# Kernel optimization log

Hardware: AMD Instinct MI355X
Metric: run time of the kernel (lower is better)

Reference implementation:

```python
import jax, jax.numpy as jnp
import numpy as np

D_MODEL = 768
N_HEADS = 12
HEAD_DIM = D_MODEL // N_HEADS
NEG = -10000.0


def setup_inputs() -> dict:
    key = jax.random.key(0)
    ks = jax.random.split(key, 8)
    B, S, D = 2, 2048, D_MODEL
    inp = {
        "q": jax.random.normal(ks[0], (B, S, D), dtype=jnp.float32),
        "k": jax.random.normal(ks[1], (B, S, D), dtype=jnp.float32),
        "v": jax.random.normal(ks[2], (B, S, D), dtype=jnp.float32),
        "attn_mask": jax.random.randint(ks[3], (B, S), 0, 2, dtype=jnp.int32),
        # weights stored [in, out]; apply as x @ W (equivalent to torch Linear)
        "Wq": jax.random.normal(ks[4], (D, D), dtype=jnp.float32) / np.sqrt(D),
        "Wk": jax.random.normal(ks[5], (D, D), dtype=jnp.float32) / np.sqrt(D),
        "Wv": jax.random.normal(ks[6], (D, D), dtype=jnp.float32) / np.sqrt(D),
        "Wo": jax.random.normal(ks[7], (D, D), dtype=jnp.float32) / np.sqrt(D),
        "mask_future": 1,
    }
    return inp


def reference(q, k, v, attn_mask, Wq, Wk, Wv, Wo, mask_future):
    B, S, D = q.shape
    H, hd = N_HEADS, HEAD_DIM
    # project and split heads -> [B, H, S, hd]
    qh = (q @ Wq).reshape(B, S, H, hd).transpose(0, 2, 1, 3)
    kh = (k @ Wk).reshape(B, S, H, hd).transpose(0, 2, 1, 3)
    vh = (v @ Wv).reshape(B, S, H, hd).transpose(0, 2, 1, 3)

    scale = 1.0 / np.sqrt(hd).astype(np.float32)
    # full [B, H, L, S] score matrix (naive SDPA, as in the original)
    scores = jnp.einsum("bhld,bhsd->bhls", qh, kh) * scale
    if mask_future:
        causal = jnp.triu(jnp.full((S, S), NEG, dtype=scores.dtype), k=1)
        scores = scores + causal
    # padding mask: [B, S] -> broadcast over heads and query positions
    pad = attn_mask[:, None, None, :] == 0
    scores = jnp.where(pad, NEG, scores)
    attn = jax.nn.softmax(scores, axis=-1)  # dropout p=0.0 -> identity
    out = jnp.einsum("bhls,bhsd->bhld", attn, vh)  # [B, H, L, hd]
    out = out.transpose(0, 2, 1, 3).reshape(B, S, D)
    return out @ Wo
```

## Files before the change

kernel.cpp:

```cpp
#include <hip/hip_runtime.h>


#define NEGV (-10000.0f)

typedef __attribute__((ext_vector_type(8))) short v8s;
typedef __attribute__((ext_vector_type(4))) float v4f;
typedef __attribute__((ext_vector_type(8))) unsigned short v8u;

#define GLDS16(g, l)                                            \
  __builtin_amdgcn_global_load_lds(                             \
      (const __attribute__((address_space(1))) void*)(g),       \
      (__attribute__((address_space(3))) void*)(l), 16, 0, 0)

__device__ __forceinline__ unsigned short f2bf(float f) {
  unsigned int u = __float_as_uint(f);
  u += 0x7FFFu + ((u >> 16) & 1u);
  return (unsigned short)(u >> 16);
}

__device__ __forceinline__ unsigned int cvt_pk_bf16(float lo, float hi) {
  unsigned int r;
  asm("v_cvt_pk_bf16_f32 %0, %1, %2" : "=v"(r) : "v"(lo), "v"(hi));
  return r;
}

__global__ __launch_bounds__(256) void transpose_w(
    const float* __restrict__ w0, const float* __restrict__ w1,
    const float* __restrict__ w2, const float* __restrict__ w3,
    unsigned short* __restrict__ t0, unsigned short* __restrict__ t1,
    unsigned short* __restrict__ t2, unsigned short* __restrict__ t3) {
  const float* w; unsigned short* t;
  switch (blockIdx.z) {
    case 0: w = w0; t = t0; break;
    case 1: w = w1; t = t1; break;
    case 2: w = w2; t = t2; break;
    default: w = w3; t = t3; break;
  }
  __shared__ unsigned short tile[32][33];
  const int tx = threadIdx.x & 31, ty = threadIdx.x >> 5;
  const int x0 = blockIdx.x * 32, y0 = blockIdx.y * 32;
#pragma unroll
  for (int j = 0; j < 4; j++)
    tile[ty + j * 8][tx] = f2bf(w[(size_t)(y0 + ty + j * 8) * 768 + x0 + tx]);
  __syncthreads();
#pragma unroll
  for (int j = 0; j < 4; j++)
    t[(size_t)(x0 + ty + j * 8) * 768 + y0 + tx] = tile[tx][ty + j * 8];
}

__global__ __launch_bounds__(256) void transpose_vh(
    const unsigned short* __restrict__ vh, unsigned short* __restrict__ vht) {
  __shared__ unsigned short tile[32][33];
  const size_t hoff = (size_t)blockIdx.z * 2048 * 64;
  const unsigned short* src = vh + hoff;
  unsigned short* dst = vht + hoff;
  const int s0 = blockIdx.x * 32, d0 = blockIdx.y * 32;
  const int tx = threadIdx.x & 31, ty = threadIdx.x >> 5;
#pragma unroll
  for (int j = 0; j < 4; j++)
    tile[ty + j * 8][tx] = src[(size_t)(s0 + ty + j * 8) * 64 + d0 + tx];
  __syncthreads();
#pragma unroll
  for (int j = 0; j < 4; j++)
    dst[(size_t)(d0 + ty + j * 8) * 2048 + s0 + tx] = tile[tx][ty + j * 8];
}

template <bool ABF16HEAD, bool CF32ROW>
__device__ __forceinline__ void gemm_core(const void* __restrict__ A,
                                          const unsigned short* __restrict__ Wt,
                                          void* __restrict__ C) {
  const int tid = threadIdx.x;
  const int wave = tid >> 6, lane = tid & 63;
  const int quad = lane >> 4, l16 = lane & 15;
  const int wm = wave >> 1, wn = wave & 1;
  const int bm = blockIdx.x * 128, bn = blockIdx.y * 128;

  __shared__ __align__(16) unsigned short As[128 * 32];
  __shared__ __align__(16) unsigned short Bs[128 * 32];

  v4f acc[4][4];
#pragma unroll
  for (int i = 0; i < 4; i++)
#pragma unroll
    for (int j = 0; j < 4; j++) acc[i][j] = (v4f){0.f, 0.f, 0.f, 0.f};

  for (int kt = 0; kt < 24; kt++) {
    __syncthreads();
#pragma unroll
    for (int p = 0; p < 2; p++) {
      int idx = p * 256 + tid;
      int r = idx >> 2, c0 = (idx & 3) << 3;
      int rg = bm + r, c = kt * 32 + c0;
      if (ABF16HEAD) {
        size_t aoff = ((size_t)((rg >> 11) * 12 + (c >> 6)) * 2048 +
                       (rg & 2047)) * 64 + (c & 63);
        GLDS16((const unsigned short*)A + aoff,
               &As[(size_t)(p * 256 + wave * 64) * 8]);
      } else {
        const float* Af = (const float*)A;
        size_t aoff = (size_t)rg * 768 + c;
        float4 x0 = *(const float4*)(Af + aoff);
        float4 x1 = *(const float4*)(Af + aoff + 4);
        v8u tmp;
        tmp[0] = f2bf(x0.x); tmp[1] = f2bf(x0.y);
        tmp[2] = f2bf(x0.z); tmp[3] = f2bf(x0.w);
        tmp[4] = f2bf(x1.x); tmp[5] = f2bf(x1.y);
        tmp[6] = f2bf(x1.z); tmp[7] = f2bf(x1.w);
        *(uint4*)&As[r * 32 + c0] = *(uint4*)&tmp;
      }
      GLDS16(&Wt[(size_t)(bn + r) * 768 + c],
             &Bs[(size_t)(p * 256 + wave * 64) * 8]);
    }
    __syncthreads();

    v8s aF[4], bF[4];
#pragma unroll
    for (int mt = 0; mt < 4; mt++)
      aF[mt] = *(const v8s*)&As[(wm * 64 + mt * 16 + l16) * 32 + quad * 8];
#pragma unroll
    for (int nt = 0; nt < 4; nt++)
      bF[nt] = *(const v8s*)&Bs[(wn * 64 + nt * 16 + l16) * 32 + quad * 8];
#pragma unroll
    for (int mt = 0; mt < 4; mt++)
#pragma unroll
      for (int nt = 0; nt < 4; nt++)
        acc[mt][nt] = __builtin_amdgcn_mfma_f32_16x16x32_bf16(
            aF[mt], bF[nt], acc[mt][nt], 0, 0, 0);
  }

#pragma unroll
  for (int mt = 0; mt < 4; mt++) {
#pragma unroll
    for (int i = 0; i < 4; i++) {
      int row = bm + wm * 64 + mt * 16 + quad * 4 + i;
#pragma unroll
      for (int nt = 0; nt < 4; nt++) {
        int col = bn + wn * 64 + nt * 16 + l16;
        if (CF32ROW) {
          ((float*)C)[(size_t)row * 768 + col] = acc[mt][nt][i];
        } else {
          size_t off = ((size_t)((row >> 11) * 12 + (col >> 6)) * 2048 +
                        (row & 2047)) * 64 + (col & 63);
          ((unsigned short*)C)[off] = f2bf(acc[mt][nt][i]);
        }
      }
    }
  }
}

__global__ __launch_bounds__(256) void gemm_qkv(
    const float* __restrict__ xq, const float* __restrict__ xk,
    const float* __restrict__ xv, const unsigned short* __restrict__ wqt,
    const unsigned short* __restrict__ wkt, const unsigned short* __restrict__ wvt,
    unsigned short* __restrict__ qh, unsigned short* __restrict__ kh,
    unsigned short* __restrict__ vh) {
  const float* A; const unsigned short* Wt; unsigned short* C;
  switch (blockIdx.z) {
    case 0: A = xq; Wt = wqt; C = qh; break;
    case 1: A = xk; Wt = wkt; C = kh; break;
    default: A = xv; Wt = wvt; C = vh; break;
  }
  gemm_core<false, false>((const void*)A, Wt, (void*)C);
}

__global__ __launch_bounds__(256) void gemm_o(
    const unsigned short* __restrict__ oat, const unsigned short* __restrict__ wot,
    float* __restrict__ out) {
  gemm_core<true, true>((const void*)oat, wot, (void*)out);
}

__global__ __launch_bounds__(256) void attn_kernel(
    const unsigned short* __restrict__ qh, const unsigned short* __restrict__ kh,
    const unsigned short* __restrict__ vht, const int* __restrict__ attn_mask,
    const int* __restrict__ mask_future, unsigned short* __restrict__ o) {
  const int S = 2048, HD = 64, NH = 12;

  const int nlin = blockIdx.x + 32 * blockIdx.y;
  const int m_ = nlin & 255, t_ = nlin >> 8;
  const int i_ = (t_ == 1) ? (511 - m_) : (t_ * 256 + m_);
  const int qt = 31 - i_ / 24;
  const int bh = i_ - (i_ / 24) * 24;
  const int b = bh / NH, h = bh % NH;

  const int tid = threadIdx.x;
  const int wave = tid >> 6, lane = tid & 63;
  const int quad = lane >> 4, l16 = lane & 15;

  __shared__ __align__(16) unsigned short Ks[2][64 * 72];
  __shared__ __align__(16) unsigned short Vt[2][64 * 72];
  __shared__ __align__(16) unsigned short Ps[4][16 * 72];
  __shared__ int s_flag;

  const size_t head_off = (size_t)(b * NH + h) * S * HD;
  const unsigned short* Kb = kh + head_off;
  const unsigned short* Vb = vht + head_off;

  const int mf = mask_future[0];
  if (tid == 0) s_flag = 0;

  const int qrow_l = qt * 64 + wave * 16 + l16;
  v8s aQ[2];
  {
    const unsigned short* qp = qh + head_off + (size_t)qrow_l * HD + quad * 8;
    aQ[0] = *(const v8s*)(qp);
    aQ[1] = *(const v8s*)(qp + 32);
  }
  const int qbase_D = qt * 64 + wave * 16 + quad * 4;

  float m_i = -1e30f;
  v4f accO[4], accL;
  accL = (v4f){0.f, 0.f, 0.f, 0.f};
#pragma unroll
  for (int dt = 0; dt < 4; dt++) accO[dt] = (v4f){0.f, 0.f, 0.f, 0.f};

  v8s ones;
#pragma unroll
  for (int j = 0; j < 8; j++) ones[j] = (short)0x3F80;

  const int kt_causal = mf ? qt : (S / 64 - 1);
  const int r0 = tid >> 3, c0s = (tid & 7) << 3;

  auto nexttile = [&](int t) -> int {
    if (t < kt_causal) return t + 1;
    if (t == kt_causal) return (mf && kt_causal < S / 64 - 1) ? t + 1 : -1;
    return (t < S / 64 - 1) ? t + 1 : -1;
  };

  uint4 pk0, pk1, pv0, pv1;
  int pmv = 0;
  unsigned long long msk0 = 0, msk1 = 0;
  int rtile = -1, stile = -1;

  auto prefetch = [&](int kt) {
    const uint4* srck = (const uint4*)(Kb + (size_t)kt * 64 * HD);
    pk0 = srck[tid];
    pk1 = srck[256 + tid];
    const unsigned short* vp = Vb + (size_t)r0 * S + kt * 64 + c0s;
    pv0 = *(const uint4*)vp;
    pv1 = *(const uint4*)(vp + (size_t)32 * S);
    pmv = attn_mask[b * S + kt * 64 + lane];
    rtile = kt;
  };

  auto stage = [&](int kb) {
    *(uint4*)&Ks[kb][r0 * 72 + c0s] = pk0;
    *(uint4*)&Ks[kb][(r0 + 32) * 72 + c0s] = pk1;
    *(uint4*)&Vt[kb][r0 * 72 + c0s] = pv0;
    *(uint4*)&Vt[kb][(r0 + 32) * 72 + c0s] = pv1;
    unsigned long long mk = __ballot(pmv != 0);
    if (kb) msk1 = mk; else msk0 = mk;
  };

  for (int phase = 0; phase < 2; phase++) {
    int kt_lo, kt_hi;
    if (phase == 0) { kt_lo = 0; kt_hi = kt_causal; }
    else {
      if (m_i < -5000.f) s_flag = 1;
      __syncthreads();
      if (!s_flag) break;
      kt_lo = kt_causal + 1; kt_hi = S / 64 - 1;
      if (kt_lo > kt_hi) break;
    }

    if (stile != kt_lo) {
      if (rtile != kt_lo) prefetch(kt_lo);
      stage(kt_lo & 1);
      stile = kt_lo;
      int nx = nexttile(kt_lo);
      if (nx >= 0) prefetch(nx);
    }

    for (int kt = kt_lo; kt <= kt_hi; kt++) {
      __syncthreads();

      int nkt = nexttile(kt);
      if (nkt >= 0 && stile != nkt) {
        stage(nkt & 1);
        stile = nkt;
        int n2 = nexttile(nkt);
        if (n2 >= 0) prefetch(n2);
      }

      const int kb = kt & 1;
      const unsigned short* KsB = Ks[kb];
      const unsigned short* VtB = Vt[kb];
      const unsigned long long mk = kb ? msk1 : msk0;

      v4f sc[4];
      __builtin_amdgcn_s_setprio(1);
#pragma unroll
      for (int nt = 0; nt < 4; nt++) {
        const unsigned short* kp = &KsB[(nt * 16 + l16) * 72 + quad * 8];
        v8s k0 = *(const v8s*)kp;
        v8s k1 = *(const v8s*)(kp + 32);
        v4f z = (v4f){0.f, 0.f, 0.f, 0.f};
        z = __builtin_amdgcn_mfma_f32_16x16x32_bf16(k0, aQ[0], z, 0, 0, 0);
        z = __builtin_amdgcn_mfma_f32_16x16x32_bf16(k1, aQ[1], z, 0, 0, 0);
        sc[nt] = z;
      }
      __builtin_amdgcn_s_setprio(0);

#pragma unroll
      for (int nt = 0; nt < 4; nt++) {
#pragma unroll
        for (int i = 0; i < 4; i++) {
          int kid = nt * 16 + quad * 4 + i;
          int key = kt * 64 + kid;
          float v = sc[nt][i] * 0.125f;
          v += (mf && (key > qrow_l)) ? NEGV : 0.f;
          v = ((mk >> kid) & 1ull) ? v : NEGV;
          sc[nt][i] = v;
        }
      }

      float mx;
      {
        float a = fmaxf(fmaxf(sc[0][0], sc[0][1]), fmaxf(sc[0][2], sc[0][3]));
        float b2 = fmaxf(fmaxf(sc[1][0], sc[1][1]), fmaxf(sc[1][2], sc[1][3]));
        float c = fmaxf(fmaxf(sc[2][0], sc[2][1]), fmaxf(sc[2][2], sc[2][3]));
        float d = fmaxf(fmaxf(sc[3][0], sc[3][1]), fmaxf(sc[3][2], sc[3][3]));
        mx = fmaxf(fmaxf(a, b2), fmaxf(c, d));
      }
      mx = fmaxf(mx, __shfl_xor(mx, 16));
      mx = fmaxf(mx, __shfl_xor(mx, 32));

      if (!__all(mx - m_i <= 8.0f)) {
        float mnew = fmaxf(m_i, mx);
        float alpha = __expf(m_i - mnew);
        m_i = mnew;
        float a0 = __shfl(alpha, quad * 4 + 0);
        float a1 = __shfl(alpha, quad * 4 + 1);
        float a2 = __shfl(alpha, quad * 4 + 2);
        float a3 = __shfl(alpha, quad * 4 + 3);
#pragma unroll
        for (int dt = 0; dt < 4; dt++) {
          accO[dt][0] *= a0; accO[dt][1] *= a1;
          accO[dt][2] *= a2; accO[dt][3] *= a3;
        }
        accL[0] *= a0; accL[1] *= a1; accL[2] *= a2; accL[3] *= a3;
      }

#pragma unroll
      for (int nt = 0; nt < 4; nt++) {
#pragma unroll
        for (int i = 0; i < 4; i++)
          sc[nt][i] = __expf(sc[nt][i] - m_i);
        uint2 w;
        w.x = cvt_pk_bf16(sc[nt][0], sc[nt][1]);
        w.y = cvt_pk_bf16(sc[nt][2], sc[nt][3]);
        *(uint2*)&Ps[wave][l16 * 72 + nt * 16 + quad * 4] = w;
      }

      __builtin_amdgcn_s_setprio(1);
#pragma unroll
      for (int ks = 0; ks < 2; ks++) {
        v8s aP = *(const v8s*)&Ps[wave][l16 * 72 + ks * 32 + quad * 8];
        accL = __builtin_amdgcn_mfma_f32_16x16x32_bf16(aP, ones, accL, 0, 0, 0);
#pragma unroll
        for (int dt = 0; dt < 4; dt++) {
          v8s bV = *(const v8s*)&VtB[(dt * 16 + l16) * 72 + ks * 32 + quad * 8];
          accO[dt] =
              __builtin_amdgcn_mfma_f32_16x16x32_bf16(aP, bV, accO[dt], 0, 0, 0);
        }
      }
      __builtin_amdgcn_s_setprio(0);
    }
    if (phase == 0) __syncthreads();
  }

#pragma unroll
  for (int i = 0; i < 4; i++) {
    float inv = 1.f / accL[i];
    int qr = qbase_D + i;
    size_t base = head_off + (size_t)qr * HD;
#pragma unroll
    for (int dt = 0; dt < 4; dt++)
      o[base + dt * 16 + l16] = f2bf(accO[dt][i] * inv);
  }
}

extern "C" void kernel_launch(void* const* d_in, const int* in_sizes, int n_in,
                              void* d_out, int out_size, void* d_ws, size_t ws_size,
                              hipStream_t stream) {
  const float* q  = (const float*)d_in[0];
  const float* k  = (const float*)d_in[1];
  const float* v  = (const float*)d_in[2];
  const int* amask = (const int*)d_in[3];
  const float* Wq = (const float*)d_in[4];
  const float* Wk = (const float*)d_in[5];
  const float* Wv = (const float*)d_in[6];
  const float* Wo = (const float*)d_in[7];
  const int* mf  = (const int*)d_in[8];
  float* out = (float*)d_out;

  unsigned short* ws = (unsigned short*)d_ws;
  unsigned short* qh = ws;
  unsigned short* kh = qh + 3145728;
  unsigned short* vh = kh + 3145728;
  unsigned short* wqt = vh + 3145728;
  unsigned short* wkt = wqt + 589824;
  unsigned short* wvt = wkt + 589824;
  unsigned short* wot = wvt + 589824;
  unsigned short* vht = (unsigned short*)d_out;

  transpose_w<<<dim3(24, 24, 4), 256, 0, stream>>>(Wq, Wk, Wv, Wo,
                                                   wqt, wkt, wvt, wot);
  gemm_qkv<<<dim3(32, 6, 3), 256, 0, stream>>>(q, k, v, wqt, wkt, wvt,
                                               qh, kh, vh);
  transpose_vh<<<dim3(64, 2, 24), 256, 0, stream>>>(vh, vht);
  attn_kernel<<<dim3(32, 24), 256, 0, stream>>>(qh, kh, vht, amask, mf, qh);
  gemm_o<<<dim3(32, 6), 256, 0, stream>>>(qh, wot, out);
}
```

Measured before the change: 212.9 us.

## Double-buffer LDS tiles in projection GEMM to overlap loads with MFMA

The projection GEMM core now keeps two LDS buffers for A and B. It issues the global loads for the next k-tile before running the MFMAs on the current tile, so the two barriers per iteration become one. For the fp32 A path, the next tile is held in registers and converted to bf16 into LDS after the compute step. This roughly doubles LDS use per block and raises register pressure, which may lower occupancy.

```diff
diff --git a/kernel.cpp b/kernel.cpp
--- a/kernel.cpp
+++ b/kernel.cpp
@@ -75,8 +75,10 @@
   const int wm = wave >> 1, wn = wave & 1;
   const int bm = blockIdx.x * 128, bn = blockIdx.y * 128;
 
-  __shared__ __align__(16) unsigned short As[128 * 32];
-  __shared__ __align__(16) unsigned short Bs[128 * 32];
+  __shared__ __align__(16) unsigned short As[2][128 * 32];
+  __shared__ __align__(16) unsigned short Bs[2][128 * 32];
+
+  const int r0s = tid >> 2, c0s = (tid & 3) << 3;
 
   v4f acc[4][4];
 #pragma unroll
@@ -84,48 +86,86 @@
 #pragma unroll
     for (int j = 0; j < 4; j++) acc[i][j] = (v4f){0.f, 0.f, 0.f, 0.f};
 
+  float4 nA00, nA01, nA10, nA11;
+
+  auto issueB = [&](int kt, int nb) {
+    const int c = kt * 32 + c0s;
+    GLDS16(&Wt[(size_t)(bn + r0s) * 768 + c],
+           &Bs[nb][(size_t)(wave * 64) * 8]);
+    GLDS16(&Wt[(size_t)(bn + r0s + 64) * 768 + c],
+           &Bs[nb][(size_t)(256 + wave * 64) * 8]);
+  };
+  auto issueA_glds = [&](int kt, int nb) {
+    const int c = kt * 32 + c0s;
+    const int rg0 = bm + r0s, rg1 = bm + r0s + 64;
+    size_t a0 = ((size_t)((rg0 >> 11) * 12 + (c >> 6)) * 2048 +
+                 (rg0 & 2047)) * 64 + (c & 63);
+    size_t a1 = ((size_t)((rg1 >> 11) * 12 + (c >> 6)) * 2048 +
+                 (rg1 & 2047)) * 64 + (c & 63);
+    GLDS16((const unsigned short*)A + a0, &As[nb][(size_t)(wave * 64) * 8]);
+    GLDS16((const unsigned short*)A + a1,
+           &As[nb][(size_t)(256 + wave * 64) * 8]);
+  };
+  auto issueA_f32 = [&](int kt) {
+    const float* Af = (const float*)A;
+    const int c = kt * 32 + c0s;
+    size_t a0 = (size_t)(bm + r0s) * 768 + c;
+    size_t a1 = (size_t)(bm + r0s + 64) * 768 + c;
+    nA00 = *(const float4*)(Af + a0);
+    nA01 = *(const float4*)(Af + a0 + 4);
+    nA10 = *(const float4*)(Af + a1);
+    nA11 = *(const float4*)(Af + a1 + 4);
+  };
+  auto writeA_f32 = [&](int nb) {
+    v8u t0, t1;
+    t0[0] = f2bf(nA00.x); t0[1] = f2bf(nA00.y);
+    t0[2] = f2bf(nA00.z); t0[3] = f2bf(nA00.w);
+    t0[4] = f2bf(nA01.x); t0[5] = f2bf(nA01.y);
+    t0[6] = f2bf(nA01.z); t0[7] = f2bf(nA01.w);
+    t1[0] = f2bf(nA10.x); t1[1] = f2bf(nA10.y);
+    t1[2] = f2bf(nA10.z); t1[3] = f2bf(nA10.w);
+    t1[4] = f2bf(nA11.x); t1[5] = f2bf(nA11.y);
+    t1[6] = f2bf(nA11.z); t1[7] = f2bf(nA11.w);
+    *(uint4*)&As[nb][r0s * 32 + c0s] = *(uint4*)&t0;
+    *(uint4*)&As[nb][(r0s + 64) * 32 + c0s] = *(uint4*)&t1;
+  };
+
+  if (ABF16HEAD) {
+    issueA_glds(0, 0);
+  } else {
+    issueA_f32(0);
+  }
+  issueB(0, 0);
+  if (!ABF16HEAD) writeA_f32(0);
+  __syncthreads();
+
   for (int kt = 0; kt < 24; kt++) {
-    __syncthreads();
-#pragma unroll
-    for (int p = 0; p < 2; p++) {
-      int idx = p * 256 + tid;
-      int r = idx >> 2, c0 = (idx & 3) << 3;
-      int rg = bm + r, c = kt * 32 + c0;
-      if (ABF16HEAD) {
-        size_t aoff = ((size_t)((rg >> 11) * 12 + (c >> 6)) * 2048 +
-                       (rg & 2047)) * 64 + (c & 63);
-        GLDS16((const unsigned short*)A + aoff,
-               &As[(size_t)(p * 256 + wave * 64) * 8]);
-      } else {
-        const float* Af = (const float*)A;
-        size_t aoff = (size_t)rg * 768 + c;
-        float4 x0 = *(const float4*)(Af + aoff);
-        float4 x1 = *(const float4*)(Af + aoff + 4);
-        v8u tmp;
-        tmp[0] = f2bf(x0.x); tmp[1] = f2bf(x0.y);
-        tmp[2] = f2bf(x0.z); tmp[3] = f2bf(x0.w);
-        tmp[4] = f2bf(x1.x); tmp[5] = f2bf(x1.y);
-        tmp[6] = f2bf(x1.z); tmp[7] = f2bf(x1.w);
-        *(uint4*)&As[r * 32 + c0] = *(uint4*)&tmp;
-      }
-      GLDS16(&Wt[(size_t)(bn + r) * 768 + c],
-             &Bs[(size_t)(p * 256 + wave * 64) * 8]);
+    const int cur = kt & 1, nxt = cur ^ 1;
+
+    if (kt < 23) {
+      if (ABF16HEAD) issueA_glds(kt + 1, nxt);
+      else issueA_f32(kt + 1);
+      issueB(kt + 1, nxt);
     }
-    __syncthreads();
 
     v8s aF[4], bF[4];
 #pragma unroll
     for (int mt = 0; mt < 4; mt++)
-      aF[mt] = *(const v8s*)&As[(wm * 64 + mt * 16 + l16) * 32 + quad * 8];
+      aF[mt] =
+          *(const v8s*)&As[cur][(wm * 64 + mt * 16 + l16) * 32 + quad * 8];
 #pragma unroll
     for (int nt = 0; nt < 4; nt++)
-      bF[nt] = *(const v8s*)&Bs[(wn * 64 + nt * 16 + l16) * 32 + quad * 8];
+      bF[nt] =
+          *(const v8s*)&Bs[cur][(wn * 64 + nt * 16 + l16) * 32 + quad * 8];
 #pragma unroll
     for (int mt = 0; mt < 4; mt++)
 #pragma unroll
       for (int nt = 0; nt < 4; nt++)
         acc[mt][nt] = __builtin_amdgcn_mfma_f32_16x16x32_bf16(
             aF[mt], bF[nt], acc[mt][nt], 0, 0, 0);
+
+    if (kt < 23 && !ABF16HEAD) writeA_f32(nxt);
+    __syncthreads();
   }
 
 #pragma unroll
```

Result: no change. 210.7 us (-1.1%).
